# Performance work log

Measured on AMD Instinct MI355X. Metric: run time of the kernel, lower is better.

## Reference

```python
import jax, jax.numpy as jnp
import numpy as np

B, IN_DIM, HID = 16384, 256, 512
DT, N_STEPS_ARG = 0.1, 1
N_SOLVER_STEPS = 8  # fixed-step dopri5 substitute for adaptive dopri5

# Dormand-Prince (dopri5) tableau (5th-order solution weights)
_A = (
    (1/5,),
    (3/40, 9/40),
    (44/45, -56/15, 32/9),
    (19372/6561, -25360/2187, 64448/6561, -212/729),
    (9017/3168, -355/33, 46732/5247, 49/176, -5103/18656),
)
_B = (35/384, 0.0, 500/1113, 125/192, -2187/6784, 11/84)


def setup_inputs() -> dict:
    key = jax.random.key(0)
    ks = jax.random.split(key, 10)
    s_in = 1.0 / np.sqrt(IN_DIM)
    s_h = 1.0 / np.sqrt(HID)
    return {
        "y": jax.random.normal(ks[0], (B, HID), jnp.float32),
        "u_t": jax.random.normal(ks[1], (B, IN_DIM), jnp.float32),
        "Wp": jax.random.uniform(ks[2], (IN_DIM, HID), jnp.float32, -s_in, s_in),
        "bp": jax.random.uniform(ks[3], (HID,), jnp.float32, -s_in, s_in),
        "W1": jax.random.uniform(ks[4], (HID, HID), jnp.float32, -s_h, s_h),
        "b1": jax.random.uniform(ks[5], (HID,), jnp.float32, -s_h, s_h),
        "W2": jax.random.uniform(ks[6], (HID, HID), jnp.float32, -s_h, s_h),
        "b2": jax.random.uniform(ks[7], (HID,), jnp.float32, -s_h, s_h),
        "W3": jax.random.uniform(ks[8], (HID, HID), jnp.float32, -s_h, s_h),
        "b3": jax.random.uniform(ks[9], (HID,), jnp.float32, -s_h, s_h),
    }


def _ode_f(y, W1, b1, W2, b2, W3, b3):
    h = jnp.tanh(y @ W1 + b1)
    h = jnp.tanh(h @ W2 + b2)
    return h @ W3 + b3


def reference(y, u_t, Wp, bp, W1, b1, W2, b2, W3, b3):
    y0 = y + (u_t @ Wp + bp)  # input projection added to state
    T = DT * N_STEPS_ARG
    h = jnp.asarray(T / N_SOLVER_STEPS, y0.dtype)
    f = lambda s: _ode_f(s, W1, b1, W2, b2, W3, b3)

    def step(s, _):
        k1 = f(s)
        k2 = f(s + h * (_A[0][0] * k1))
        k3 = f(s + h * (_A[1][0] * k1 + _A[1][1] * k2))
        k4 = f(s + h * (_A[2][0] * k1 + _A[2][1] * k2 + _A[2][2] * k3))
        k5 = f(s + h * (_A[3][0] * k1 + _A[3][1] * k2 + _A[3][2] * k3 + _A[3][3] * k4))
        k6 = f(s + h * (_A[4][0] * k1 + _A[4][1] * k2 + _A[4][2] * k3 + _A[4][3] * k4 + _A[4][4] * k5))
        s_next = s + h * (_B[0] * k1 + _B[2] * k3 + _B[3] * k4 + _B[4] * k5 + _B[5] * k6)
        return s_next, None

    y_final, _ = jax.lax.scan(step, y0, None, length=N_SOLVER_STEPS)
    return y_final
```

## Files before the change

kernel.cpp:

```cpp
#include <hip/hip_runtime.h>
#include <hip/hip_bf16.h>
#include <cstddef>

typedef unsigned short u16;
typedef short bf16x8 __attribute__((ext_vector_type(8)));
typedef float f32x4 __attribute__((ext_vector_type(4)));
typedef unsigned short u16x8 __attribute__((ext_vector_type(8)));
typedef unsigned short u16x4 __attribute__((ext_vector_type(4)));

#define MDIM 16384
#define NDIM 512
#define HPAD 520

__device__ __forceinline__ float b2f(u16 u) {
    return __uint_as_float(((unsigned int)u) << 16);
}
__device__ __forceinline__ u16 f2b(float f) {
    unsigned int x = __float_as_uint(f);
    x += 0x7fffu + ((x >> 16) & 1u);
    return (u16)(x >> 16);
}
__device__ __forceinline__ float fast_tanh(float x) {
    float e = __expf(2.0f * x);
    return 1.0f - 2.0f * __builtin_amdgcn_rcpf(e + 1.0f);
}

template <int KDIM, int EPI, bool AF32>
__global__ __launch_bounds__(256, 2) void gemm_bt(
    const void* __restrict__ Avoid, const u16* __restrict__ Bt,
    const float* __restrict__ bias, const float* __restrict__ addf,
    u16* __restrict__ Cb, float* __restrict__ Cf) {
    __shared__ u16 As[128 * 72];
    __shared__ u16 Bs[128 * 72];
    const int tid = threadIdx.x;
    const int m0 = blockIdx.y * 128;
    const int n0 = blockIdx.x * 128;
    const int lane = tid & 63;
    const int wave = tid >> 6;
    const int wm = (wave & 1) * 64;
    const int wn = (wave >> 1) * 64;
    const int lr = lane & 15;
    const int lk = (lane >> 4) * 8;

    f32x4 acc[4][4];
    f32x4 zero = {0.0f, 0.0f, 0.0f, 0.0f};
#pragma unroll
    for (int i = 0; i < 4; ++i)
#pragma unroll
        for (int j = 0; j < 4; ++j) acc[i][j] = zero;

    const int r0 = tid >> 3;
    const int c0 = (tid & 7) * 8;

    for (int kt = 0; kt < KDIM / 64; ++kt) {
        const int k0 = kt * 64;
#pragma unroll
        for (int it = 0; it < 4; ++it) {
            int r = it * 32 + r0;
            if constexpr (AF32) {
                const float* Af = (const float*)Avoid;
                const float* src = Af + (size_t)(m0 + r) * KDIM + k0 + c0;
                f32x4 lo = *(const f32x4*)(src);
                f32x4 hi = *(const f32x4*)(src + 4);
                u16x8 t;
#pragma unroll
                for (int q = 0; q < 4; ++q) { t[q] = f2b(lo[q]); t[q + 4] = f2b(hi[q]); }
                *(u16x8*)(&As[r * 72 + c0]) = t;
            } else {
                const u16* Ab = (const u16*)Avoid;
                *(f32x4*)(&As[r * 72 + c0]) =
                    *(const f32x4*)(Ab + (size_t)(m0 + r) * KDIM + k0 + c0);
            }
            *(f32x4*)(&Bs[r * 72 + c0]) =
                *(const f32x4*)(Bt + (size_t)(n0 + r) * KDIM + k0 + c0);
        }
        __syncthreads();
#pragma unroll
        for (int kk = 0; kk < 2; ++kk) {
            bf16x8 af[4], bw[4];
#pragma unroll
            for (int i = 0; i < 4; ++i) {
                af[i] = __builtin_bit_cast(
                    bf16x8, *(const f32x4*)(&As[(wm + i * 16 + lr) * 72 + kk * 32 + lk]));
                bw[i] = __builtin_bit_cast(
                    bf16x8, *(const f32x4*)(&Bs[(wn + i * 16 + lr) * 72 + kk * 32 + lk]));
            }
#pragma unroll
            for (int i = 0; i < 4; ++i)
#pragma unroll
                for (int j = 0; j < 4; ++j)
                    acc[i][j] = __builtin_amdgcn_mfma_f32_16x16x32_bf16(
                        af[i], bw[j], acc[i][j], 0, 0, 0);
        }
        __syncthreads();
    }
#pragma unroll
    for (int j = 0; j < 4; ++j) {
        const int col = n0 + wn + j * 16 + lr;
        const float bv = bias[col];
#pragma unroll
        for (int i = 0; i < 4; ++i) {
            const int rowb = m0 + wm + i * 16 + (lane >> 4) * 4;
#pragma unroll
            for (int r = 0; r < 4; ++r) {
                float v = acc[i][j][r] + bv;
                size_t off = (size_t)(rowb + r) * NDIM + col;
                if constexpr (EPI == 0) {
                    v += addf[off];
                    Cf[off] = v;
                    Cb[off] = f2b(v);
                }
                if constexpr (EPI == 1) Cb[off] = f2b(tanhf(v));
                if constexpr (EPI == 2) Cb[off] = f2b(v);
                if constexpr (EPI == 3) {
                    v += addf[off];
                    Cf[off] = v;
                }
            }
        }
    }
}

template <int NT, bool WS>
__global__ __launch_bounds__(512, 2) void ode_eval(
    const float* __restrict__ S32, float* __restrict__ S32out,
    const u16* __restrict__ P1, const u16* __restrict__ P2,
    const u16* __restrict__ P3, const u16* __restrict__ P4,
    const u16* __restrict__ P5,
    float c1, float c2, float c3, float c4, float c5,
    const u16* __restrict__ W1t, const float* __restrict__ bb1,
    const u16* __restrict__ W2t, const float* __restrict__ bb2,
    const u16* __restrict__ W3t, const float* __restrict__ bb3,
    u16* __restrict__ Kout) {
    __shared__ u16 As[64 * HPAD];
    __shared__ u16 Hs[64 * HPAD];
    const int tid = threadIdx.x;
    const int lane = tid & 63;
    const int wn = (tid >> 6) * 64;
    const int lr = lane & 15;
    const int lk = (lane >> 4) * 8;
    const size_t row0 = (size_t)blockIdx.x * 64;

    {
        const u16* kp[5] = {P1, P2, P3, P4, P5};
        const float cs[5] = {c1, c2, c3, c4, c5};
#pragma unroll 2
        for (int it = tid; it < 4096; it += 512) {
            const int r = it >> 6;
            const int c8 = (it & 63) << 3;
            const size_t g = (row0 + r) * 512 + c8;
            f32x4 lo = *(const f32x4*)(S32 + g);
            f32x4 hi = *(const f32x4*)(S32 + g + 4);
#pragma unroll
            for (int t = 0; t < NT; ++t) {
                u16x8 v = *(const u16x8*)(kp[t] + g);
#pragma unroll
                for (int q = 0; q < 4; ++q) {
                    lo[q] += cs[t] * b2f(v[q]);
                    hi[q] += cs[t] * b2f(v[q + 4]);
                }
            }
            if constexpr (WS) {
                *(f32x4*)(S32out + g) = lo;
                *(f32x4*)(S32out + g + 4) = hi;
            }
            u16x8 o;
#pragma unroll
            for (int q = 0; q < 4; ++q) { o[q] = f2b(lo[q]); o[q + 4] = f2b(hi[q]); }
            *(u16x8*)(&As[r * HPAD + c8]) = o;
        }
    }
    __syncthreads();

#define MLP_LAYER(SRC, WT, BIAS, DST, DO_TANH)                                     \
    {                                                                              \
        f32x4 acc[4][4];                                                           \
        _Pragma("unroll") for (int i = 0; i < 4; ++i)                              \
            _Pragma("unroll") for (int j = 0; j < 4; ++j)                          \
                acc[i][j] = (f32x4){0.0f, 0.0f, 0.0f, 0.0f};                       \
        _Pragma("unroll 4") for (int kt = 0; kt < 16; ++kt) {                      \
            bf16x8 af[4], bw[4];                                                   \
            _Pragma("unroll") for (int j = 0; j < 4; ++j)                          \
                bw[j] = __builtin_bit_cast(bf16x8,                                 \
                    *(const f32x4*)(WT + (size_t)((wn + j * 16 + lr) << 9) +       \
                                    kt * 32 + lk));                                \
            _Pragma("unroll") for (int i = 0; i < 4; ++i)                          \
                af[i] = __builtin_bit_cast(bf16x8,                                 \
                    *(const f32x4*)(&SRC[(i * 16 + lr) * HPAD + kt * 32 + lk]));   \
            _Pragma("unroll") for (int i = 0; i < 4; ++i)                          \
                _Pragma("unroll") for (int j = 0; j < 4; ++j)                      \
                    acc[i][j] = __builtin_amdgcn_mfma_f32_16x16x32_bf16(           \
                        af[i], bw[j], acc[i][j], 0, 0, 0);                         \
        }                                                                          \
        _Pragma("unroll") for (int j = 0; j < 4; ++j) {                            \
            const float bv = BIAS[wn + j * 16 + lr];                               \
            _Pragma("unroll") for (int i = 0; i < 4; ++i) {                        \
                const int rb = i * 16 + ((lane >> 4) << 2);                        \
                _Pragma("unroll") for (int r = 0; r < 4; ++r) {                    \
                    float v = acc[i][j][r] + bv;                                   \
                    if (DO_TANH) v = fast_tanh(v);                                 \
                    DST[(rb + r) * HPAD + wn + j * 16 + lr] = f2b(v);              \
                }                                                                  \
            }                                                                      \
        }                                                                          \
    }

    MLP_LAYER(As, W1t, bb1, Hs, true);
    __syncthreads();
    MLP_LAYER(Hs, W2t, bb2, As, true);
    __syncthreads();
    MLP_LAYER(As, W3t, bb3, Hs, false);
    __syncthreads();
#undef MLP_LAYER

#pragma unroll 2
    for (int it = tid; it < 4096; it += 512) {
        const int r = it >> 6;
        const int c8 = (it & 63) << 3;
        *(f32x4*)(Kout + (row0 + r) * 512 + c8) = *(const f32x4*)(&Hs[r * HPAD + c8]);
    }
}

__global__ void transpose_k(const float* __restrict__ in, u16* __restrict__ out,
                            int R, int Ncols) {
    int idx = blockIdx.x * 256 + threadIdx.x;
    int r = idx / Ncols, c = idx % Ncols;
    out[(size_t)c * R + r] = f2b(in[idx]);
}

__global__ __launch_bounds__(256) void combo(
    const float* __restrict__ S32,
    const u16* __restrict__ p1, const u16* __restrict__ p2,
    const u16* __restrict__ p3, const u16* __restrict__ p4,
    const u16* __restrict__ p5,
    float c1, float c2, float c3, float c4, float c5, int nterms,
    float* __restrict__ outF, u16* __restrict__ outB) {
    size_t off = ((size_t)blockIdx.x * 256 + threadIdx.x) * 4;
    f32x4 a = *(const f32x4*)(S32 + off);
    const u16* ps[5] = {p1, p2, p3, p4, p5};
    float cs[5] = {c1, c2, c3, c4, c5};
    for (int t = 0; t < nterms; ++t) {
        u16x4 v = *(const u16x4*)(ps[t] + off);
#pragma unroll
        for (int i = 0; i < 4; ++i) a[i] += cs[t] * b2f(v[i]);
    }
    if (outF) *(f32x4*)(outF + off) = a;
    if (outB) {
        u16x4 o;
#pragma unroll
        for (int i = 0; i < 4; ++i) o[i] = f2b(a[i]);
        *(u16x4*)(outB + off) = o;
    }
}

extern "C" void kernel_launch(void* const* d_in, const int* in_sizes, int n_in,
                              void* d_out, int out_size, void* d_ws, size_t ws_size,
                              hipStream_t stream) {
    const float *y = nullptr, *u_t = nullptr, *Wp = nullptr, *bp = nullptr;
    const float *W1 = nullptr, *b1 = nullptr, *W2 = nullptr, *b2 = nullptr;
    const float *W3 = nullptr, *b3 = nullptr;
    {
        const float* w262[3] = {nullptr, nullptr, nullptr};
        const float* s512[4] = {nullptr, nullptr, nullptr, nullptr};
        int i512[4] = {0, 0, 0, 0};
        int n262 = 0, n512 = 0;
        for (int i = 0; i < n_in; ++i) {
            const float* p = (const float*)d_in[i];
            int sz = in_sizes[i];
            if (sz == MDIM * NDIM) y = p;
            else if (sz == MDIM * 256) u_t = p;
            else if (sz == 256 * 512) Wp = p;
            else if (sz == 512 * 512) { if (n262 < 3) w262[n262++] = p; }
            else if (sz == 512) { if (n512 < 4) { i512[n512] = i; s512[n512++] = p; } }
        }
        W1 = w262[0]; W2 = w262[1]; W3 = w262[2];
        bool contig = (n512 == 4) && (i512[3] == i512[0] + 3);
        if (contig) { b1 = s512[0]; b2 = s512[1]; b3 = s512[2]; bp = s512[3]; }
        else        { bp = s512[0]; b1 = s512[1]; b2 = s512[2]; b3 = s512[3]; }
        if (!y || !u_t || !Wp || !W1 || n512 < 4) {
            y  = (const float*)d_in[0]; u_t = (const float*)d_in[1];
            Wp = (const float*)d_in[2]; bp  = (const float*)d_in[3];
            W1 = (const float*)d_in[4]; b1  = (const float*)d_in[5];
            W2 = (const float*)d_in[6]; b2  = (const float*)d_in[7];
            W3 = (const float*)d_in[8]; b3  = (const float*)d_in[9];
        }
    }

    u16* ws  = (u16*)d_ws;
    u16* Wpt = ws;
    u16* W1t = Wpt + 512 * 256;
    u16* W2t = W1t + 512 * 512;
    u16* W3t = W2t + 512 * 512;
    const size_t wfix = 512 * 256 + 3 * 512 * 512;

    long wsElems = (long)(ws_size / 2);
    long chunk = (wsElems - (long)wfix) / (7L * NDIM);
    chunk = (chunk / 128) * 128;
    if (chunk > MDIM) chunk = MDIM;
    if (chunk < 128) chunk = 128;

    transpose_k<<<512, 256, 0, stream>>>(Wp, Wpt, 256, 512);
    transpose_k<<<1024, 256, 0, stream>>>(W1, W1t, 512, 512);
    transpose_k<<<1024, 256, 0, stream>>>(W2, W2t, 512, 512);
    transpose_k<<<1024, 256, 0, stream>>>(W3, W3t, 512, 512);

    const double h = 0.1 / 8.0;
    const float A21 = (float)(h * 1.0 / 5.0);
    const float A31 = (float)(h * 3.0 / 40.0),      A32 = (float)(h * 9.0 / 40.0);
    const float A41 = (float)(h * 44.0 / 45.0),     A42 = (float)(h * -56.0 / 15.0);
    const float A43 = (float)(h * 32.0 / 9.0);
    const float A51 = (float)(h * 19372.0 / 6561.0),A52 = (float)(h * -25360.0 / 2187.0);
    const float A53 = (float)(h * 64448.0 / 6561.0),A54 = (float)(h * -212.0 / 729.0);
    const float A61 = (float)(h * 9017.0 / 3168.0), A62 = (float)(h * -355.0 / 33.0);
    const float A63 = (float)(h * 46732.0 / 5247.0),A64 = (float)(h * 49.0 / 176.0);
    const float A65 = (float)(h * -5103.0 / 18656.0);
    const float B1c = (float)(h * 35.0 / 384.0),    B3c = (float)(h * 500.0 / 1113.0);
    const float B4c = (float)(h * 125.0 / 192.0),   B5c = (float)(h * -2187.0 / 6784.0);
    const float B6c = (float)(h * 11.0 / 84.0);

    float* OUT = (float*)d_out;

    for (long row0 = 0; row0 < MDIM; row0 += chunk) {
        const long rows = (MDIM - row0 < chunk) ? (MDIM - row0) : chunk;
        const size_t CB = (size_t)rows * NDIM;

        u16* base = ws + wfix;
        float* S32 = (float*)base;
        u16* K1 = base + 2 * CB;
        u16* K2 = base + 3 * CB;
        u16* K3 = base + 4 * CB;
        u16* K4 = base + 5 * CB;
        u16* K5 = base + 6 * CB;
        u16* K6 = K2;

        dim3 gg(4, (unsigned)(rows / 128));
        gemm_bt<256, 3, true><<<gg, 256, 0, stream>>>(
            (const void*)(u_t + (size_t)row0 * 256), Wpt, bp,
            y + (size_t)row0 * NDIM, nullptr, S32);

        const int nb = (int)(rows / 64);
        for (int st = 0; st < 8; ++st) {
            if (st == 0)
                ode_eval<0, false><<<nb, 512, 0, stream>>>(
                    S32, nullptr, nullptr, nullptr, nullptr, nullptr, nullptr,
                    0.f, 0.f, 0.f, 0.f, 0.f,
                    W1t, b1, W2t, b2, W3t, b3, K1);
            else
                ode_eval<5, true><<<nb, 512, 0, stream>>>(
                    S32, S32, K1, K3, K4, K5, K6,
                    B1c, B3c, B4c, B5c, B6c,
                    W1t, b1, W2t, b2, W3t, b3, K1);
            ode_eval<1, false><<<nb, 512, 0, stream>>>(
                S32, nullptr, K1, nullptr, nullptr, nullptr, nullptr,
                A21, 0.f, 0.f, 0.f, 0.f,
                W1t, b1, W2t, b2, W3t, b3, K2);
            ode_eval<2, false><<<nb, 512, 0, stream>>>(
                S32, nullptr, K1, K2, nullptr, nullptr, nullptr,
                A31, A32, 0.f, 0.f, 0.f,
                W1t, b1, W2t, b2, W3t, b3, K3);
            ode_eval<3, false><<<nb, 512, 0, stream>>>(
                S32, nullptr, K1, K2, K3, nullptr, nullptr,
                A41, A42, A43, 0.f, 0.f,
                W1t, b1, W2t, b2, W3t, b3, K4);
            ode_eval<4, false><<<nb, 512, 0, stream>>>(
                S32, nullptr, K1, K2, K3, K4, nullptr,
                A51, A52, A53, A54, 0.f,
                W1t, b1, W2t, b2, W3t, b3, K5);
            ode_eval<5, false><<<nb, 512, 0, stream>>>(
                S32, nullptr, K1, K2, K3, K4, K5,
                A61, A62, A63, A64, A65,
                W1t, b1, W2t, b2, W3t, b3, K6);
        }
        const int NC = (int)(CB / 4 / 256);
        combo<<<NC, 256, 0, stream>>>(S32, K1, K3, K4, K5, K6,
            B1c, B3c, B4c, B5c, B6c, 5,
            OUT + (size_t)row0 * NDIM, nullptr);
    }
}
```

Before: 3.325 ms.

## Fuse all dopri5 stages and steps into one persistent per-tile kernel

Replaces the 48 per-stage ode_eval launches plus the final combo kernel with a single kernel in which each 64-row block runs all 8 steps and 6 stages. The fp32 state is held in registers instead of being reread and rewritten in global memory, and K6 stays in shared memory for the final update. This removes launch overhead and state traffic, but adds register pressure from the 64-float state array, which could cause spills at launch bounds 512,2. K1-K5 are still exchanged through global memory within the block.

```diff
diff --git a/kernel.cpp b/kernel.cpp
--- a/kernel.cpp
+++ b/kernel.cpp
@@ -105,12 +105,6 @@
             for (int r = 0; r < 4; ++r) {
                 float v = acc[i][j][r] + bv;
                 size_t off = (size_t)(rowb + r) * NDIM + col;
-                if constexpr (EPI == 0) {
-                    v += addf[off];
-                    Cf[off] = v;
-                    Cb[off] = f2b(v);
-                }
-                if constexpr (EPI == 1) Cb[off] = f2b(tanhf(v));
                 if constexpr (EPI == 2) Cb[off] = f2b(v);
                 if constexpr (EPI == 3) {
                     v += addf[off];
@@ -121,17 +115,58 @@
     }
 }
 
-template <int NT, bool WS>
-__global__ __launch_bounds__(512, 2) void ode_eval(
-    const float* __restrict__ S32, float* __restrict__ S32out,
-    const u16* __restrict__ P1, const u16* __restrict__ P2,
-    const u16* __restrict__ P3, const u16* __restrict__ P4,
-    const u16* __restrict__ P5,
-    float c1, float c2, float c3, float c4, float c5,
+template <int NT>
+__device__ __forceinline__ void stage_to_As(
+    float (&Sreg)[8][8], u16* As, size_t row0, int rown, int c8,
+    const u16* p1, const u16* p2, const u16* p3, const u16* p4, const u16* p5,
+    float c1, float c2, float c3, float c4, float c5) {
+#pragma unroll
+    for (int k = 0; k < 8; ++k) {
+        const int r = rown + k * 8;
+        const size_t g = (row0 + r) * 512 + c8;
+        float v[8];
+#pragma unroll
+        for (int q = 0; q < 8; ++q) v[q] = Sreg[k][q];
+        if constexpr (NT >= 1) {
+            u16x8 kv = *(const u16x8*)(p1 + g);
+#pragma unroll
+            for (int q = 0; q < 8; ++q) v[q] += c1 * b2f(kv[q]);
+        }
+        if constexpr (NT >= 2) {
+            u16x8 kv = *(const u16x8*)(p2 + g);
+#pragma unroll
+            for (int q = 0; q < 8; ++q) v[q] += c2 * b2f(kv[q]);
+        }
+        if constexpr (NT >= 3) {
+            u16x8 kv = *(const u16x8*)(p3 + g);
+#pragma unroll
+            for (int q = 0; q < 8; ++q) v[q] += c3 * b2f(kv[q]);
+        }
+        if constexpr (NT >= 4) {
+            u16x8 kv = *(const u16x8*)(p4 + g);
+#pragma unroll
+            for (int q = 0; q < 8; ++q) v[q] += c4 * b2f(kv[q]);
+        }
+        if constexpr (NT >= 5) {
+            u16x8 kv = *(const u16x8*)(p5 + g);
+#pragma unroll
+            for (int q = 0; q < 8; ++q) v[q] += c5 * b2f(kv[q]);
+        }
+        u16x8 o;
+#pragma unroll
+        for (int q = 0; q < 8; ++q) o[q] = f2b(v[q]);
+        *(u16x8*)(&As[r * HPAD + c8]) = o;
+    }
+}
+
+__global__ __launch_bounds__(512, 2) void ode_mega(
+    const float* __restrict__ S32,
     const u16* __restrict__ W1t, const float* __restrict__ bb1,
     const u16* __restrict__ W2t, const float* __restrict__ bb2,
     const u16* __restrict__ W3t, const float* __restrict__ bb3,
-    u16* __restrict__ Kout) {
+    u16* __restrict__ K1, u16* __restrict__ K2, u16* __restrict__ K3,
+    u16* __restrict__ K4, u16* __restrict__ K5,
+    float* __restrict__ OUT) {
     __shared__ u16 As[64 * HPAD];
     __shared__ u16 Hs[64 * HPAD];
     const int tid = threadIdx.x;
@@ -140,37 +175,30 @@
     const int lr = lane & 15;
     const int lk = (lane >> 4) * 8;
     const size_t row0 = (size_t)blockIdx.x * 64;
-
-    {
-        const u16* kp[5] = {P1, P2, P3, P4, P5};
-        const float cs[5] = {c1, c2, c3, c4, c5};
-#pragma unroll 2
-        for (int it = tid; it < 4096; it += 512) {
-            const int r = it >> 6;
-            const int c8 = (it & 63) << 3;
-            const size_t g = (row0 + r) * 512 + c8;
-            f32x4 lo = *(const f32x4*)(S32 + g);
-            f32x4 hi = *(const f32x4*)(S32 + g + 4);
-#pragma unroll
-            for (int t = 0; t < NT; ++t) {
-                u16x8 v = *(const u16x8*)(kp[t] + g);
-#pragma unroll
-                for (int q = 0; q < 4; ++q) {
-                    lo[q] += cs[t] * b2f(v[q]);
-                    hi[q] += cs[t] * b2f(v[q + 4]);
-                }
-            }
-            if constexpr (WS) {
-                *(f32x4*)(S32out + g) = lo;
-                *(f32x4*)(S32out + g + 4) = hi;
-            }
-            u16x8 o;
-#pragma unroll
-            for (int q = 0; q < 4; ++q) { o[q] = f2b(lo[q]); o[q + 4] = f2b(hi[q]); }
-            *(u16x8*)(&As[r * HPAD + c8]) = o;
-        }
-    }
-    __syncthreads();
+    const int rown = tid >> 6;
+    const int c8 = (tid & 63) << 3;
+
+    constexpr double h = 0.1 / 8.0;
+    constexpr float A21 = (float)(h * 1.0 / 5.0);
+    constexpr float A31 = (float)(h * 3.0 / 40.0), A32 = (float)(h * 9.0 / 40.0);
+    constexpr float A41 = (float)(h * 44.0 / 45.0), A42 = (float)(h * -56.0 / 15.0);
+    constexpr float A43 = (float)(h * 32.0 / 9.0);
+    constexpr float A51 = (float)(h * 19372.0 / 6561.0), A52 = (float)(h * -25360.0 / 2187.0);
+    constexpr float A53 = (float)(h * 64448.0 / 6561.0), A54 = (float)(h * -212.0 / 729.0);
+    constexpr float A61 = (float)(h * 9017.0 / 3168.0), A62 = (float)(h * -355.0 / 33.0);
+    constexpr float A63 = (float)(h * 46732.0 / 5247.0), A64 = (float)(h * 49.0 / 176.0);
+    constexpr float A65 = (float)(h * -5103.0 / 18656.0);
+    constexpr float B1c = (float)(h * 35.0 / 384.0), B3c = (float)(h * 500.0 / 1113.0);
+    constexpr float B4c = (float)(h * 125.0 / 192.0), B5c = (float)(h * -2187.0 / 6784.0);
+    constexpr float B6c = (float)(h * 11.0 / 84.0);
+
+    float Sreg[8][8];
+#pragma unroll
+    for (int k = 0; k < 8; ++k) {
+        const size_t g = (row0 + rown + k * 8) * 512 + c8;
+        *(f32x4*)&Sreg[k][0] = *(const f32x4*)(S32 + g);
+        *(f32x4*)&Sreg[k][4] = *(const f32x4*)(S32 + g + 4);
+    }
 
 #define MLP_LAYER(SRC, WT, BIAS, DST, DO_TANH)                                     \
     {                                                                              \
@@ -205,20 +233,123 @@
         }                                                                          \
     }
 
-    MLP_LAYER(As, W1t, bb1, Hs, true);
-    __syncthreads();
-    MLP_LAYER(Hs, W2t, bb2, As, true);
-    __syncthreads();
-    MLP_LAYER(As, W3t, bb3, Hs, false);
-    __syncthreads();
+    for (int st = 0; st < 8; ++st) {
+        for (int e = 0; e < 6; ++e) {
+            if (e == 0)
+                stage_to_As<0>(Sreg, As, row0, rown, c8,
+                               nullptr, nullptr, nullptr, nullptr, nullptr,
+                               0.f, 0.f, 0.f, 0.f, 0.f);
+            else if (e == 1)
+                stage_to_As<1>(Sreg, As, row0, rown, c8,
+                               K1, nullptr, nullptr, nullptr, nullptr,
+                               A21, 0.f, 0.f, 0.f, 0.f);
+            else if (e == 2)
+                stage_to_As<2>(Sreg, As, row0, rown, c8,
+                               K1, K2, nullptr, nullptr, nullptr,
+                               A31, A32, 0.f, 0.f, 0.f);
+            else if (e == 3)
+                stage_to_As<3>(Sreg, As, row0, rown, c8,
+                               K1, K2, K3, nullptr, nullptr,
+                               A41, A42, A43, 0.f, 0.f);
+            else if (e == 4)
+                stage_to_As<4>(Sreg, As, row0, rown, c8,
+                               K1, K2, K3, K4, nullptr,
+                               A51, A52, A53, A54, 0.f);
+            else
+                stage_to_As<5>(Sreg, As, row0, rown, c8,
+                               K1, K2, K3, K4, K5,
+                               A61, A62, A63, A64, A65);
+            __syncthreads();
+
+            MLP_LAYER(As, W1t, bb1, Hs, true);
+            __syncthreads();
+            MLP_LAYER(Hs, W2t, bb2, As, true);
+            __syncthreads();
+
+            f32x4 acc3[4][4];
+#pragma unroll
+            for (int i = 0; i < 4; ++i)
+#pragma unroll
+                for (int j = 0; j < 4; ++j) acc3[i][j] = (f32x4){0.f, 0.f, 0.f, 0.f};
+#pragma unroll 4
+            for (int kt = 0; kt < 16; ++kt) {
+                bf16x8 af[4], bw[4];
+#pragma unroll
+                for (int j = 0; j < 4; ++j)
+                    bw[j] = __builtin_bit_cast(bf16x8,
+                        *(const f32x4*)(W3t + (size_t)((wn + j * 16 + lr) << 9) +
+                                        kt * 32 + lk));
+#pragma unroll
+                for (int i = 0; i < 4; ++i)
+                    af[i] = __builtin_bit_cast(bf16x8,
+                        *(const f32x4*)(&As[(i * 16 + lr) * HPAD + kt * 32 + lk]));
+#pragma unroll
+                for (int i = 0; i < 4; ++i)
+#pragma unroll
+                    for (int j = 0; j < 4; ++j)
+                        acc3[i][j] = __builtin_amdgcn_mfma_f32_16x16x32_bf16(
+                            af[i], bw[j], acc3[i][j], 0, 0, 0);
+            }
+#pragma unroll
+            for (int j = 0; j < 4; ++j) {
+                const float bv = bb3[wn + j * 16 + lr];
+#pragma unroll
+                for (int i = 0; i < 4; ++i)
+#pragma unroll
+                    for (int r = 0; r < 4; ++r) acc3[i][j][r] += bv;
+            }
+
+            if (e < 5) {
+                u16* kd = (e == 0) ? K1 : (e == 1) ? K2 : (e == 2) ? K3
+                        : (e == 3) ? K4 : K5;
+#pragma unroll
+                for (int j = 0; j < 4; ++j) {
+                    const int col = wn + j * 16 + lr;
+#pragma unroll
+                    for (int i = 0; i < 4; ++i) {
+                        const int rb = i * 16 + ((lane >> 4) << 2);
+#pragma unroll
+                        for (int r = 0; r < 4; ++r)
+                            kd[(row0 + rb + r) * 512 + col] = f2b(acc3[i][j][r]);
+                    }
+                }
+                __syncthreads();
+            } else {
+#pragma unroll
+                for (int j = 0; j < 4; ++j) {
+                    const int col = wn + j * 16 + lr;
+#pragma unroll
+                    for (int i = 0; i < 4; ++i) {
+                        const int rb = i * 16 + ((lane >> 4) << 2);
+#pragma unroll
+                        for (int r = 0; r < 4; ++r)
+                            Hs[(rb + r) * HPAD + col] = f2b(acc3[i][j][r]);
+                    }
+                }
+                __syncthreads();
+#pragma unroll
+                for (int k = 0; k < 8; ++k) {
+                    const int r = rown + k * 8;
+                    const size_t g = (row0 + r) * 512 + c8;
+                    u16x8 v1 = *(const u16x8*)(K1 + g);
+                    u16x8 v3 = *(const u16x8*)(K3 + g);
+                    u16x8 v4 = *(const u16x8*)(K4 + g);
+                    u16x8 v5 = *(const u16x8*)(K5 + g);
+                    u16x8 v6 = *(const u16x8*)(&Hs[r * HPAD + c8]);
+#pragma unroll
+                    for (int q = 0; q < 8; ++q)
+                        Sreg[k][q] += B1c * b2f(v1[q]) + B3c * b2f(v3[q]) +
+                                      B4c * b2f(v4[q]) + B5c * b2f(v5[q]) +
+                                      B6c * b2f(v6[q]);
+                    if (st == 7) {
+                        *(f32x4*)(OUT + g) = *(f32x4*)&Sreg[k][0];
+                        *(f32x4*)(OUT + g + 4) = *(f32x4*)&Sreg[k][4];
+                    }
+                }
+            }
+        }
+    }
 #undef MLP_LAYER
-
-#pragma unroll 2
-    for (int it = tid; it < 4096; it += 512) {
-        const int r = it >> 6;
-        const int c8 = (it & 63) << 3;
-        *(f32x4*)(Kout + (row0 + r) * 512 + c8) = *(const f32x4*)(&Hs[r * HPAD + c8]);
-    }
 }
 
 __global__ void transpose_k(const float* __restrict__ in, u16* __restrict__ out,
@@ -226,31 +357,6 @@
     int idx = blockIdx.x * 256 + threadIdx.x;
     int r = idx / Ncols, c = idx % Ncols;
     out[(size_t)c * R + r] = f2b(in[idx]);
-}
-
-__global__ __launch_bounds__(256) void combo(
-    const float* __restrict__ S32,
-    const u16* __restrict__ p1, const u16* __restrict__ p2,
-    const u16* __restrict__ p3, const u16* __restrict__ p4,
-    const u16* __restrict__ p5,
-    float c1, float c2, float c3, float c4, float c5, int nterms,
-    float* __restrict__ outF, u16* __restrict__ outB) {
-    size_t off = ((size_t)blockIdx.x * 256 + threadIdx.x) * 4;
-    f32x4 a = *(const f32x4*)(S32 + off);
-    const u16* ps[5] = {p1, p2, p3, p4, p5};
-    float cs[5] = {c1, c2, c3, c4, c5};
-    for (int t = 0; t < nterms; ++t) {
-        u16x4 v = *(const u16x4*)(ps[t] + off);
-#pragma unroll
-        for (int i = 0; i < 4; ++i) a[i] += cs[t] * b2f(v[i]);
-    }
-    if (outF) *(f32x4*)(outF + off) = a;
-    if (outB) {
-        u16x4 o;
-#pragma unroll
-        for (int i = 0; i < 4; ++i) o[i] = f2b(a[i]);
-        *(u16x4*)(outB + off) = o;
-    }
 }
 
 extern "C" void kernel_launch(void* const* d_in, const int* in_sizes, int n_in,
@@ -304,20 +410,6 @@
     transpose_k<<<1024, 256, 0, stream>>>(W2, W2t, 512, 512);
     transpose_k<<<1024, 256, 0, stream>>>(W3, W3t, 512, 512);
 
-    const double h = 0.1 / 8.0;
-    const float A21 = (float)(h * 1.0 / 5.0);
-    const float A31 = (float)(h * 3.0 / 40.0),      A32 = (float)(h * 9.0 / 40.0);
-    const float A41 = (float)(h * 44.0 / 45.0),     A42 = (float)(h * -56.0 / 15.0);
-    const float A43 = (float)(h * 32.0 / 9.0);
-    const float A51 = (float)(h * 19372.0 / 6561.0),A52 = (float)(h * -25360.0 / 2187.0);
-    const float A53 = (float)(h * 64448.0 / 6561.0),A54 = (float)(h * -212.0 / 729.0);
-    const float A61 = (float)(h * 9017.0 / 3168.0), A62 = (float)(h * -355.0 / 33.0);
-    const float A63 = (float)(h * 46732.0 / 5247.0),A64 = (float)(h * 49.0 / 176.0);
-    const float A65 = (float)(h * -5103.0 / 18656.0);
-    const float B1c = (float)(h * 35.0 / 384.0),    B3c = (float)(h * 500.0 / 1113.0);
-    const float B4c = (float)(h * 125.0 / 192.0),   B5c = (float)(h * -2187.0 / 6784.0);
-    const float B6c = (float)(h * 11.0 / 84.0);
-
     float* OUT = (float*)d_out;
 
     for (long row0 = 0; row0 < MDIM; row0 += chunk) {
@@ -331,7 +423,6 @@
         u16* K3 = base + 4 * CB;
         u16* K4 = base + 5 * CB;
         u16* K5 = base + 6 * CB;
-        u16* K6 = K2;
 
         dim3 gg(4, (unsigned)(rows / 128));
         gemm_bt<256, 3, true><<<gg, 256, 0, stream>>>(
@@ -339,41 +430,9 @@
             y + (size_t)row0 * NDIM, nullptr, S32);
 
         const int nb = (int)(rows / 64);
-        for (int st = 0; st < 8; ++st) {
-            if (st == 0)
-                ode_eval<0, false><<<nb, 512, 0, stream>>>(
-                    S32, nullptr, nullptr, nullptr, nullptr, nullptr, nullptr,
-                    0.f, 0.f, 0.f, 0.f, 0.f,
-                    W1t, b1, W2t, b2, W3t, b3, K1);
-            else
-                ode_eval<5, true><<<nb, 512, 0, stream>>>(
-                    S32, S32, K1, K3, K4, K5, K6,
-                    B1c, B3c, B4c, B5c, B6c,
-                    W1t, b1, W2t, b2, W3t, b3, K1);
-            ode_eval<1, false><<<nb, 512, 0, stream>>>(
-                S32, nullptr, K1, nullptr, nullptr, nullptr, nullptr,
-                A21, 0.f, 0.f, 0.f, 0.f,
-                W1t, b1, W2t, b2, W3t, b3, K2);
-            ode_eval<2, false><<<nb, 512, 0, stream>>>(
-                S32, nullptr, K1, K2, nullptr, nullptr, nullptr,
-                A31, A32, 0.f, 0.f, 0.f,
-                W1t, b1, W2t, b2, W3t, b3, K3);
-            ode_eval<3, false><<<nb, 512, 0, stream>>>(
-                S32, nullptr, K1, K2, K3, nullptr, nullptr,
-                A41, A42, A43, 0.f, 0.f,
-                W1t, b1, W2t, b2, W3t, b3, K4);
-            ode_eval<4, false><<<nb, 512, 0, stream>>>(
-                S32, nullptr, K1, K2, K3, K4, nullptr,
-                A51, A52, A53, A54, 0.f,
-                W1t, b1, W2t, b2, W3t, b3, K5);
-            ode_eval<5, false><<<nb, 512, 0, stream>>>(
-                S32, nullptr, K1, K2, K3, K4, K5,
-                A61, A62, A63, A64, A65,
-                W1t, b1, W2t, b2, W3t, b3, K6);
-        }
-        const int NC = (int)(CB / 4 / 256);
-        combo<<<NC, 256, 0, stream>>>(S32, K1, K3, K4, K5, K6,
-            B1c, B3c, B4c, B5c, B6c, 5,
-            OUT + (size_t)row0 * NDIM, nullptr);
-    }
-}
+        ode_mega<<<nb, 512, 0, stream>>>(
+            S32, W1t, b1, W2t, b2, W3t, b3,
+            K1, K2, K3, K4, K5,
+            OUT + (size_t)row0 * NDIM);
+    }
+}
```

After: 3.071 ms. 7.6% less time.
